# Performance work log

Measured on AMD Instinct MI355X. Metric: run time of the kernel, lower is better.

## Reference

```python
import jax, jax.numpy as jnp
import numpy as np

B, H, W, C = 2, 64, 64, 512
GROUPS = 32
EPS = 1e-5


def group_norm(x, gamma, beta):
    b, h, w, c = x.shape
    xg = x.reshape(b, h, w, GROUPS, c // GROUPS)
    mu = xg.mean(axis=(1, 2, 4), keepdims=True)
    var = xg.var(axis=(1, 2, 4), keepdims=True)
    xn = ((xg - mu) * jax.lax.rsqrt(var + EPS)).reshape(b, h, w, c)
    return xn * gamma + beta


def setup_inputs() -> dict:
    key = jax.random.key(0)
    ks = jax.random.split(key, 12)
    wscale = 0.02
    inputs = jax.random.normal(ks[0], (B, H, W, C), jnp.float32)
    gamma = jnp.ones((C,), jnp.float32)
    beta = jnp.zeros((C,), jnp.float32)
    Wq = jax.random.normal(ks[1], (C, C), jnp.float32) * wscale
    bq = jnp.zeros((C,), jnp.float32)
    Wk = jax.random.normal(ks[2], (C, C), jnp.float32) * wscale
    bk = jnp.zeros((C,), jnp.float32)
    Wv = jax.random.normal(ks[3], (C, C), jnp.float32) * wscale
    bv = jnp.zeros((C,), jnp.float32)
    Wp = jax.random.normal(ks[4], (C, C), jnp.float32) * wscale
    bp = jnp.zeros((C,), jnp.float32)
    return {"inputs": inputs, "gamma": gamma, "beta": beta,
            "Wq": Wq, "bq": bq, "Wk": Wk, "bk": bk,
            "Wv": Wv, "bv": bv, "Wp": Wp, "bp": bp}


def reference(inputs, gamma, beta, Wq, bq, Wk, bk, Wv, bv, Wp, bp):
    b, h, w, c = inputs.shape
    x = group_norm(inputs, gamma, beta)
    # QKV projections on [b, h, w, c], flatten spatial to sequence hw
    q = (x @ Wq + bq).reshape(b, h * w, c)
    k = (x @ Wk + bk).reshape(b, h * w, c)
    v = (x @ Wv + bv).reshape(b, h * w, c)
    scale = 1.0 / jnp.sqrt(jnp.asarray(c, q.dtype))
    # y[b,i,j] = <q_i, k_j> / sqrt(c); softmax over keys j (last axis, keras default)
    attn = jax.nn.softmax(jnp.einsum('bqc,bkc->bqk', q, k) * scale, axis=-1)
    # out_i = sum_j attn[i,j] * v_j  (matches v @ y^T in the original)
    o = jnp.einsum('bqk,bkc->bqc', attn, v).reshape(b, h, w, c)
    return (o @ Wp + bp) + inputs
```

## Files before the change

### kernel.cpp

```cpp
#include <hip/hip_runtime.h>
#include <hip/hip_bf16.h>
#include <hip/hip_cooperative_groups.h>
#include <cstddef>

namespace cg = cooperative_groups;


typedef __bf16 bf16;
typedef __attribute__((ext_vector_type(8))) __bf16 bf16x8;
typedef __attribute__((ext_vector_type(4))) __bf16 bf16x4;
typedef __attribute__((ext_vector_type(4))) float f32x4;

#define SEQ   4096
#define CCH   512
#define NBAT  2
#define NOMASK 0x7FFFFFFF
#define SMEM_BYTES 32768

__device__ __forceinline__ void prep_unit(
    char* smem, int bid, const float* __restrict__ x,
    const float* __restrict__ Wq, const float* __restrict__ Wk,
    const float* __restrict__ Wv, const float* __restrict__ Wp,
    const float* __restrict__ bq, const float* __restrict__ bk,
    const float* __restrict__ bv,
    float* __restrict__ statsP, bf16* __restrict__ WqkvT,
    bf16* __restrict__ WpT, float* __restrict__ biasQKV) {
    const int tid = threadIdx.x;
    if (bid < 512) {
        float* red = (float*)smem;
        int bg = bid >> 3, c = bid & 7;
        int b = bg >> 5, g = bg & 31;
        const float* base = x + (size_t)b * SEQ * CCH + g * 16;
        float s = 0.f, ss = 0.f;
        for (int i = tid; i < 2048; i += 256) {
            int sp = c * 512 + (i >> 2), q = i & 3;
            float4 v = *(const float4*)(base + (size_t)sp * CCH + q * 4);
            s  += v.x + v.y + v.z + v.w;
            ss += v.x * v.x + v.y * v.y + v.z * v.z + v.w * v.w;
        }
        #pragma unroll
        for (int o = 32; o > 0; o >>= 1) { s += __shfl_down(s, o); ss += __shfl_down(ss, o); }
        int wave = tid >> 6, lane = tid & 63;
        if (lane == 0) { red[wave] = s; red[4 + wave] = ss; }
        __syncthreads();
        if (tid == 0) {
            statsP[bg * 16 + c]     = red[0] + red[1] + red[2] + red[3];
            statsP[bg * 16 + 8 + c] = red[4] + red[5] + red[6] + red[7];
        }
        __syncthreads();
    } else if (bid < 1536) {
        float (*tile)[33] = (float(*)[33])smem;
        int w = bid - 512;
        int z = w >> 8, rest = w & 255;
        int k0 = (rest >> 4) * 32, n0 = (rest & 15) * 32;
        const float* W = (z == 0) ? Wq : (z == 1) ? Wk : (z == 2) ? Wv : Wp;
        int tx = tid & 31, ty = tid >> 5;
        #pragma unroll
        for (int i = ty; i < 32; i += 8)
            tile[i][tx] = W[(size_t)(k0 + i) * CCH + n0 + tx];
        __syncthreads();
        bf16* dst = (z < 3) ? (WqkvT + (size_t)z * CCH * CCH) : WpT;
        #pragma unroll
        for (int i = ty; i < 32; i += 8)
            dst[(size_t)(n0 + i) * CCH + k0 + tx] = (bf16)tile[tx][i];
        __syncthreads();
    } else {
        for (int i = tid; i < 1536; i += 256) {
            float v = (i < 512) ? bq[i] : (i < 1024) ? bk[i - 512] : bv[i - 1024];
            biasQKV[i] = v;
        }
    }
}

__device__ __forceinline__ void gn_table(char* smem, const float* __restrict__ statsP) {
    float* tbl = (float*)smem;
    const int tid = threadIdx.x;
    if (tid < 64) {
        float S = 0.f, SS = 0.f;
        #pragma unroll
        for (int c = 0; c < 8; ++c) { S += statsP[tid * 16 + c]; SS += statsP[tid * 16 + 8 + c]; }
        float mu = S * (1.f / 65536.f);
        float rs = rsqrtf(SS * (1.f / 65536.f) - mu * mu + 1e-5f);
        tbl[tid * 2] = mu; tbl[tid * 2 + 1] = rs;
    }
    __syncthreads();
}

__device__ __forceinline__ void gn_unit(
    char* smem, int w, const float* __restrict__ x,
    const float* __restrict__ gamma, const float* __restrict__ beta,
    bf16* __restrict__ xn) {
    const float* tbl = (const float*)smem;
    size_t idx = (size_t)w * 256 + threadIdx.x;
    int c4 = (int)(idx & 127);
    int b = (int)(idx >> 19);
    int bg = b * 32 + (c4 >> 2);
    float mu = tbl[bg * 2], rs = tbl[bg * 2 + 1];
    float4 v  = ((const float4*)x)[idx];
    float4 gm = ((const float4*)gamma)[c4];
    float4 bt = ((const float4*)beta)[c4];
    bf16x4 o;
    o[0] = (bf16)((v.x - mu) * rs * gm.x + bt.x);
    o[1] = (bf16)((v.y - mu) * rs * gm.y + bt.y);
    o[2] = (bf16)((v.z - mu) * rs * gm.z + bt.z);
    o[3] = (bf16)((v.w - mu) * rs * gm.w + bt.w);
    ((bf16x4*)xn)[idx] = o;
}

__device__ __forceinline__ void vtrans_unit(char* smem,
                                            const bf16* __restrict__ qkv,
                                            bf16* __restrict__ vT,
                                            int b, int s0, int c0) {
    bf16 (*tile)[65] = (bf16(*)[65])smem;
    const int tx = threadIdx.x & 63;
    const int w = threadIdx.x >> 6;
    #pragma unroll
    for (int i = 0; i < 16; ++i) {
        int row = w + i * 4;
        tile[row][tx] = qkv[((size_t)b * SEQ + s0 + row) * 1536 + 1024 + c0 + tx];
    }
    __syncthreads();
    #pragma unroll
    for (int i = 0; i < 16; ++i) {
        int row = w + i * 4;
        vT[((size_t)b * CCH + c0 + row) * SEQ + s0 + tx] = tile[tx][row];
    }
    __syncthreads();
}

template <int EPI, int BN>
__device__ __forceinline__ void gemm2_body(
    char* smem, int bxi, int byi, int bzi,
    const bf16* __restrict__ A, long long aBatch, int lda,
    const bf16* __restrict__ Bt, long long bBatch, int ldb,
    void* __restrict__ Cout, long long cBatch, int ldc,
    int K, int bkmask, float scale,
    const float* __restrict__ bias, const float* __restrict__ resid,
    float* __restrict__ lsum, long long lsumBatch) {
    constexpr int JN = BN / 32;
    bf16* As = (bf16*)smem;
    bf16* Bs = (bf16*)(smem + 16384);
    const int tid = threadIdx.x;
    const int lane = tid & 63;
    const int wave = tid >> 6;

    int zb = bzi, kc = 0;
    if constexpr (EPI == 2) { kc = zb & 1; zb >>= 1; }
    const long long m0 = (long long)bxi * 128;
    const long long n0 = (long long)byi * BN;
    const bf16* Ab = A + (long long)zb * aBatch + (EPI == 2 ? (long long)kc * 2048 : 0);
    const bf16* Bb = Bt + (long long)zb * bBatch + (EPI == 2 ? (long long)kc * 2048 : 0);

    const int wm = (wave & 1) * 64;
    const int wn = (wave >> 1) * (BN / 2);
    const int fm = lane & 15;
    const int q4 = lane >> 4;

    f32x4 acc[4][JN];
    #pragma unroll
    for (int i = 0; i < 4; ++i)
        #pragma unroll
        for (int j = 0; j < JN; ++j)
            acc[i][j] = (f32x4){0.f, 0.f, 0.f, 0.f};

    const int srow = tid >> 3;
    const int schunk = (tid & 7) ^ (srow & 7);

    for (int k0 = 0; k0 < K; k0 += 64) {
        const int kA = k0 + schunk * 8;
        const int kB = (k0 & bkmask) + schunk * 8;
        #pragma unroll
        for (int cb = 0; cb < 4; ++cb) {
            const bf16* g = Ab + (m0 + cb * 32 + srow) * (long long)lda + kA;
            __builtin_amdgcn_global_load_lds((const __attribute__((address_space(1))) void*)g,
                                             (__attribute__((address_space(3))) void*)&As[cb * 2048 + tid * 8], 16, 0, 0);
        }
        #pragma unroll
        for (int cb = 0; cb < BN / 32; ++cb) {
            const bf16* g = Bb + (n0 + cb * 32 + srow) * (long long)ldb + kB;
            __builtin_amdgcn_global_load_lds((const __attribute__((address_space(1))) void*)g,
                                             (__attribute__((address_space(3))) void*)&Bs[cb * 2048 + tid * 8], 16, 0, 0);
        }
        __syncthreads();
        #pragma unroll
        for (int kcc = 0; kcc < 2; ++kcc) {
            bf16x8 fa[4], fb[JN];
            #pragma unroll
            for (int i = 0; i < 4; ++i) {
                const int row = wm + i * 16 + fm;
                const int sw = ((kcc * 4 + q4) ^ (fm & 7)) * 8;
                fa[i] = *(const bf16x8*)&As[row * 64 + sw];
            }
            #pragma unroll
            for (int j = 0; j < JN; ++j) {
                const int row = wn + j * 16 + fm;
                const int sw = ((kcc * 4 + q4) ^ (fm & 7)) * 8;
                fb[j] = *(const bf16x8*)&Bs[row * 64 + sw];
            }
            #pragma unroll
            for (int i = 0; i < 4; ++i)
                #pragma unroll
                for (int j = 0; j < JN; ++j)
                    acc[i][j] = __builtin_amdgcn_mfma_f32_16x16x32_bf16(fa[i], fb[j], acc[i][j], 0, 0, 0);
        }
        __syncthreads();
    }

    float* lrow = (float*)(smem + 1024);
    if constexpr (EPI == 2) {
        float* lscr = (float*)smem;
        const float* lsb = lsum + (long long)zb * lsumBatch + m0;
        const int row = tid & 127, h = tid >> 7;
        float s = 0.f;
        #pragma unroll
        for (int p = 0; p < 32; ++p)
            s += lsb[(long long)(h * 32 + p) * SEQ + row];
        lscr[tid] = s;
        __syncthreads();
        if (tid < 128) lrow[tid] = 1.f / (lscr[tid] + lscr[tid + 128]);
        __syncthreads();
    }

    const int col = lane & 15;
    const int rowb = (lane >> 4) * 4;

    if constexpr (EPI == 1) {
        bf16* Pb = (bf16*)Cout + (long long)zb * cBatch;
        float* lsw = lsum + (long long)zb * lsumBatch
                   + ((long long)byi * 2 + (wave >> 1)) * SEQ;
        #pragma unroll
        for (int i = 0; i < 4; ++i) {
            float rs[4] = {0.f, 0.f, 0.f, 0.f};
            long long mg = m0 + wm + i * 16 + rowb;
            #pragma unroll
            for (int j = 0; j < JN; ++j) {
                long long ng = n0 + wn + j * 16 + col;
                #pragma unroll
                for (int r = 0; r < 4; ++r) {
                    float e = __expf(acc[i][j][r] * scale);
                    rs[r] += e;
                    Pb[(mg + r) * (long long)ldc + ng] = (bf16)e;
                }
            }
            #pragma unroll
            for (int r = 0; r < 4; ++r) {
                rs[r] += __shfl_xor(rs[r], 1);
                rs[r] += __shfl_xor(rs[r], 2);
                rs[r] += __shfl_xor(rs[r], 4);
                rs[r] += __shfl_xor(rs[r], 8);
            }
            if (col == 0) {
                #pragma unroll
                for (int r = 0; r < 4; ++r) lsw[mg + r] = rs[r];
            }
        }
    } else {
        #pragma unroll
        for (int i = 0; i < 4; ++i) {
            #pragma unroll
            for (int j = 0; j < JN; ++j) {
                long long mg = m0 + wm + i * 16 + rowb;
                long long ng = n0 + wn + j * 16 + col;
                #pragma unroll
                for (int r = 0; r < 4; ++r) {
                    float v = acc[i][j][r];
                    long long m = mg + r;
                    if constexpr (EPI == 0) {
                        ((bf16*)Cout)[m * (long long)ldc + ng] = (bf16)(v + bias[ng]);
                    } else if constexpr (EPI == 2) {
                        float inv = lrow[(int)(m - m0)];
                        ((bf16*)Cout)[(long long)zb * cBatch + m * (long long)ldc
                                      + kc * 512 + ng] = (bf16)(v * inv);
                    } else {
                        ((float*)Cout)[m * (long long)ldc + ng] =
                            v + bias[ng] + resid[m * CCH + ng];
                    }
                }
            }
        }
    }
}

struct FusedArgs {
    const float *x, *gamma, *beta, *Wq, *bq, *Wk, *bk, *Wv, *bv, *Wp, *bp;
    float* out;
    float* statsP; float* biasQKV; bf16* WqkvT; bf16* WpT; bf16* xn;
    float* lsum; bf16* qkv; bf16* o2; bf16* vT; bf16* P;
};

__global__ __launch_bounds__(256, 2) void fused(FusedArgs a) {
    cg::grid_group grid = cg::this_grid();
    __shared__ __align__(16) char smem[SMEM_BYTES];
    const int nb = gridDim.x;
    const float scale = 0.044194173824159216f;

    for (int w = blockIdx.x; w < 1537; w += nb)
        prep_unit(smem, w, a.x, a.Wq, a.Wk, a.Wv, a.Wp, a.bq, a.bk, a.bv,
                  a.statsP, a.WqkvT, a.WpT, a.biasQKV);
    grid.sync();

    gn_table(smem, a.statsP);
    for (int w = blockIdx.x; w < 4096; w += nb)
        gn_unit(smem, w, a.x, a.gamma, a.beta, a.xn);
    grid.sync();

    for (int w = blockIdx.x; w < 768; w += nb)
        gemm2_body<0, 128>(smem, w & 63, w >> 6, 0,
                           a.xn, 0, CCH, a.WqkvT, 0, CCH, a.qkv, 0, 1536,
                           CCH, NOMASK, 1.f, a.biasQKV, nullptr, nullptr, 0);
    grid.sync();

    for (int w = blockIdx.x; w < 3072; w += nb) {
        if (w < 1024) {
            int b = w >> 9, r = w & 511;
            vtrans_unit(smem, a.qkv, a.vT, b, (r >> 3) * 64, (r & 7) * 64);
        } else {
            int u = w - 1024;
            int bz = u >> 10, r = u & 1023;
            gemm2_body<1, 128>(smem, r >> 5, r & 31, bz,
                               a.qkv, (long long)SEQ * 1536, 1536,
                               a.qkv + 512, (long long)SEQ * 1536, 1536,
                               a.P, (long long)SEQ * SEQ, SEQ,
                               CCH, NOMASK, scale, nullptr, nullptr,
                               a.lsum, 64LL * SEQ);
        }
    }
    grid.sync();

    for (int w = blockIdx.x; w < 512; w += nb)
        gemm2_body<2, 128>(smem, w & 31, (w >> 5) & 3, w >> 7,
                           a.P, (long long)SEQ * SEQ, SEQ,
                           a.vT, (long long)CCH * SEQ, SEQ,
                           a.o2, (long long)SEQ * 1024, 1024,
                           2048, NOMASK, 1.f, nullptr, nullptr,
                           a.lsum, 64LL * SEQ);
    grid.sync();

    for (int w = blockIdx.x; w < 512; w += nb)
        gemm2_body<3, 64>(smem, w & 63, w >> 6, 0,
                          a.o2, 0, 1024, a.WpT, 0, CCH, a.out, 0, CCH,
                          1024, 511, 1.f, a.bp, a.x, nullptr, 0);
}

__global__ __launch_bounds__(256) void k_prep(
    const float* x, const float* Wq, const float* Wk, const float* Wv,
    const float* Wp, const float* bq, const float* bk, const float* bv,
    float* statsP, bf16* WqkvT, bf16* WpT, float* biasQKV) {
    __shared__ __align__(16) char smem[4352];
    prep_unit(smem, blockIdx.x, x, Wq, Wk, Wv, Wp, bq, bk, bv,
              statsP, WqkvT, WpT, biasQKV);
}

__global__ __launch_bounds__(256) void k_gn(
    const float* x, const float* statsP, const float* gamma,
    const float* beta, bf16* xn) {
    __shared__ __align__(16) char smem[512];
    gn_table(smem, statsP);
    gn_unit(smem, blockIdx.x, x, gamma, beta, xn);
}

template <int EPI, int BN>
__global__ __launch_bounds__(256, 2) void k_gemm2(
    const bf16* A, long long aBatch, int lda,
    const bf16* Bt, long long bBatch, int ldb,
    void* Cout, long long cBatch, int ldc,
    int K, int bkmask, float scale,
    const float* bias, const float* resid,
    float* lsum, long long lsumBatch) {
    __shared__ __align__(16) char smem[SMEM_BYTES];
    gemm2_body<EPI, BN>(smem, blockIdx.x, blockIdx.y, blockIdx.z,
                        A, aBatch, lda, Bt, bBatch, ldb, Cout, cBatch, ldc,
                        K, bkmask, scale, bias, resid, lsum, lsumBatch);
}

__global__ __launch_bounds__(256, 2) void k_qk_vtrans(
    const bf16* qkv, bf16* vT, bf16* P, float* lsum, float scale,
    int vtBlocks, long long qkBatch, long long pBatch, long long lsumBatch) {
    __shared__ __align__(16) char smem[SMEM_BYTES];
    const int bid = blockIdx.x;
    if (bid < vtBlocks) {
        int b = bid >> 9, r = bid & 511;
        vtrans_unit(smem, qkv, vT, b, (r >> 3) * 64, (r & 7) * 64);
    } else {
        int q = bid - vtBlocks;
        int bz = q >> 10, r = q & 1023;
        gemm2_body<1, 128>(smem, r >> 5, r & 31, bz,
                           qkv, qkBatch, 1536, qkv + 512, qkBatch, 1536,
                           P, pBatch, SEQ, CCH, NOMASK, scale,
                           nullptr, nullptr, lsum, lsumBatch);
    }
}

extern "C" void kernel_launch(void* const* d_in, const int* in_sizes, int n_in,
                              void* d_out, int out_size, void* d_ws, size_t ws_size,
                              hipStream_t stream) {
    const float* x     = (const float*)d_in[0];
    const float* gamma = (const float*)d_in[1];
    const float* beta  = (const float*)d_in[2];
    const float* Wq    = (const float*)d_in[3];
    const float* bq    = (const float*)d_in[4];
    const float* Wk    = (const float*)d_in[5];
    const float* bk    = (const float*)d_in[6];
    const float* Wv    = (const float*)d_in[7];
    const float* bv    = (const float*)d_in[8];
    const float* Wp    = (const float*)d_in[9];
    const float* bp    = (const float*)d_in[10];
    float* out = (float*)d_out;

    constexpr size_t OFF_STATS = 0;
    constexpr size_t OFF_BIAS  = 4096;
    constexpr size_t OFF_WQKVT = 12288;
    constexpr size_t OFF_WPT   = 1585152;
    constexpr size_t OFF_XN    = 2109440;
    constexpr size_t OFF_LSUM  = OFF_XN;
    constexpr size_t OFF_QKV   = 10498048;
    constexpr size_t OFF_O2    = OFF_QKV;
    constexpr size_t OFF_VT    = 35663872;
    constexpr size_t OFF_P     = 44052480;
    constexpr size_t NEED_FULL = OFF_P + (size_t)NBAT * SEQ * SEQ * 2;

    char* ws = (char*)d_ws;
    float* statsP  = (float*)(ws + OFF_STATS);
    float* biasQKV = (float*)(ws + OFF_BIAS);
    bf16*  WqkvT   = (bf16*)(ws + OFF_WQKVT);
    bf16*  WpT     = (bf16*)(ws + OFF_WPT);
    bf16*  xn      = (bf16*)(ws + OFF_XN);
    float* lsum    = (float*)(ws + OFF_LSUM);
    bf16*  qkv     = (bf16*)(ws + OFF_QKV);
    bf16*  o2      = (bf16*)(ws + OFF_O2);
    bf16*  vT      = (bf16*)(ws + OFF_VT);
    bf16*  P       = (bf16*)(ws + OFF_P);

    const float scale = 0.044194173824159216f;
    const bool full = ws_size >= NEED_FULL;

    bool coop = false;
    if (full) {
        int occ = 0;
        hipError_t oe = hipOccupancyMaxActiveBlocksPerMultiprocessor(
            &occ, (const void*)fused, 256, 0);
        if (oe == hipSuccess && occ >= 2) {
            FusedArgs a{x, gamma, beta, Wq, bq, Wk, bk, Wv, bv, Wp, bp, out,
                        statsP, biasQKV, WqkvT, WpT, xn, lsum, qkv, o2, vT, P};
            void* params[] = {&a};
            hipError_t le = hipLaunchCooperativeKernel(
                (const void*)fused, dim3(512), dim3(256), params, 0, stream);
            if (le == hipSuccess) coop = true;
            else (void)hipGetLastError();
        } else {
            (void)hipGetLastError();
        }
    }

    if (!coop) {
        k_prep<<<1537, 256, 0, stream>>>(x, Wq, Wk, Wv, Wp, bq, bk, bv,
                                         statsP, WqkvT, WpT, biasQKV);
        k_gn<<<4096, 256, 0, stream>>>(x, statsP, gamma, beta, xn);
        k_gemm2<0, 128><<<dim3(64, 12, 1), 256, 0, stream>>>(
            xn, 0, CCH, WqkvT, 0, CCH, qkv, 0, 1536,
            CCH, NOMASK, 1.f, biasQKV, nullptr, nullptr, 0);
        if (full) {
            k_qk_vtrans<<<3072, 256, 0, stream>>>(
                qkv, vT, P, lsum, scale, 1024,
                (long long)SEQ * 1536, (long long)SEQ * SEQ, 64LL * SEQ);
            k_gemm2<2, 128><<<dim3(32, 4, NBAT * 2), 256, 0, stream>>>(
                P, (long long)SEQ * SEQ, SEQ, vT, (long long)CCH * SEQ, SEQ,
                o2, (long long)SEQ * 1024, 1024,
                2048, NOMASK, 1.f, nullptr, nullptr, lsum, 64LL * SEQ);
        } else {
            for (int b = 0; b < NBAT; ++b) {
                const bf16* qb = qkv + (long long)b * SEQ * 1536;
                k_qk_vtrans<<<1536, 256, 0, stream>>>(
                    qb, vT + (long long)b * CCH * SEQ, P,
                    lsum + (long long)b * 64 * SEQ, scale, 512, 0, 0, 0);
                k_gemm2<2, 128><<<dim3(32, 4, 2), 256, 0, stream>>>(
                    P, 0, SEQ, vT + (long long)b * CCH * SEQ, 0, SEQ,
                    o2 + (long long)b * SEQ * 1024, 0, 1024,
                    2048, NOMASK, 1.f, nullptr, nullptr,
                    lsum + (long long)b * 64 * SEQ, 0);
            }
        }
        k_gemm2<3, 64><<<dim3(64, 8, 1), 256, 0, stream>>>(
            o2, 0, 1024, WpT, 0, CCH, out, 0, CCH,
            1024, 511, 1.f, bp, x, nullptr, 0);
    }
}
```

Before: 216.6 us.

## Replace cooperative launch with persistent kernel and custom atomic grid barrier

Swaps the cooperative-groups kernel and grid.sync for a regular launch of 1024 persistent blocks (4 per CU via launch bounds), synchronised by hand-written atomic counter barriers in workspace that are reset with a memset before each launch. The PV GEMM stage moves to 64-wide tiles with twice as many work units to fill the larger grid. The aim is to remove cooperative-launch overhead and raise occupancy. The risks are that the barrier deadlocks if not all 1024 blocks are co-resident, and that the 4-blocks-per-CU bound adds register pressure.

```diff
diff --git a/kernel.cpp b/kernel.cpp
--- a/kernel.cpp
+++ b/kernel.cpp
@@ -1,9 +1,6 @@
 #include <hip/hip_runtime.h>
 #include <hip/hip_bf16.h>
-#include <hip/hip_cooperative_groups.h>
 #include <cstddef>
-
-namespace cg = cooperative_groups;
 
 
 typedef __bf16 bf16;
@@ -16,6 +13,21 @@
 #define NBAT  2
 #define NOMASK 0x7FFFFFFF
 #define SMEM_BYTES 32768
+#define PGRID 1024
+
+__device__ __forceinline__ void grid_bar(unsigned* bar, int idx) {
+    __syncthreads();
+    if (threadIdx.x == 0) {
+        __threadfence();
+        __hip_atomic_fetch_add(&bar[idx], 1u, __ATOMIC_RELEASE,
+                               __HIP_MEMORY_SCOPE_AGENT);
+        while (__hip_atomic_load(&bar[idx], __ATOMIC_RELAXED,
+                                 __HIP_MEMORY_SCOPE_AGENT) < (unsigned)PGRID)
+            __builtin_amdgcn_s_sleep(1);
+        __threadfence();
+    }
+    __syncthreads();
+}
 
 __device__ __forceinline__ void prep_unit(
     char* smem, int bid, const float* __restrict__ x,
@@ -286,29 +298,29 @@
     float* out;
     float* statsP; float* biasQKV; bf16* WqkvT; bf16* WpT; bf16* xn;
     float* lsum; bf16* qkv; bf16* o2; bf16* vT; bf16* P;
+    unsigned* bar;
 };
 
-__global__ __launch_bounds__(256, 2) void fused(FusedArgs a) {
-    cg::grid_group grid = cg::this_grid();
+__global__ __launch_bounds__(256, 4) void persistent(FusedArgs a) {
     __shared__ __align__(16) char smem[SMEM_BYTES];
-    const int nb = gridDim.x;
+    const int nb = PGRID;
     const float scale = 0.044194173824159216f;
 
     for (int w = blockIdx.x; w < 1537; w += nb)
         prep_unit(smem, w, a.x, a.Wq, a.Wk, a.Wv, a.Wp, a.bq, a.bk, a.bv,
                   a.statsP, a.WqkvT, a.WpT, a.biasQKV);
-    grid.sync();
+    grid_bar(a.bar, 0);
 
     gn_table(smem, a.statsP);
     for (int w = blockIdx.x; w < 4096; w += nb)
         gn_unit(smem, w, a.x, a.gamma, a.beta, a.xn);
-    grid.sync();
+    grid_bar(a.bar, 1);
 
     for (int w = blockIdx.x; w < 768; w += nb)
         gemm2_body<0, 128>(smem, w & 63, w >> 6, 0,
                            a.xn, 0, CCH, a.WqkvT, 0, CCH, a.qkv, 0, 1536,
                            CCH, NOMASK, 1.f, a.biasQKV, nullptr, nullptr, 0);
-    grid.sync();
+    grid_bar(a.bar, 2);
 
     for (int w = blockIdx.x; w < 3072; w += nb) {
         if (w < 1024) {
@@ -325,16 +337,16 @@
                                a.lsum, 64LL * SEQ);
         }
     }
-    grid.sync();
-
-    for (int w = blockIdx.x; w < 512; w += nb)
-        gemm2_body<2, 128>(smem, w & 31, (w >> 5) & 3, w >> 7,
-                           a.P, (long long)SEQ * SEQ, SEQ,
-                           a.vT, (long long)CCH * SEQ, SEQ,
-                           a.o2, (long long)SEQ * 1024, 1024,
-                           2048, NOMASK, 1.f, nullptr, nullptr,
-                           a.lsum, 64LL * SEQ);
-    grid.sync();
+    grid_bar(a.bar, 3);
+
+    for (int w = blockIdx.x; w < 1024; w += nb)
+        gemm2_body<2, 64>(smem, w & 31, (w >> 5) & 7, w >> 8,
+                          a.P, (long long)SEQ * SEQ, SEQ,
+                          a.vT, (long long)CCH * SEQ, SEQ,
+                          a.o2, (long long)SEQ * 1024, 1024,
+                          2048, NOMASK, 1.f, nullptr, nullptr,
+                          a.lsum, 64LL * SEQ);
+    grid_bar(a.bar, 4);
 
     for (int w = blockIdx.x; w < 512; w += nb)
         gemm2_body<3, 64>(smem, w & 63, w >> 6, 0,
@@ -409,6 +421,7 @@
 
     constexpr size_t OFF_STATS = 0;
     constexpr size_t OFF_BIAS  = 4096;
+    constexpr size_t OFF_BAR   = 10240;
     constexpr size_t OFF_WQKVT = 12288;
     constexpr size_t OFF_WPT   = 1585152;
     constexpr size_t OFF_XN    = 2109440;
@@ -422,6 +435,7 @@
     char* ws = (char*)d_ws;
     float* statsP  = (float*)(ws + OFF_STATS);
     float* biasQKV = (float*)(ws + OFF_BIAS);
+    unsigned* bar  = (unsigned*)(ws + OFF_BAR);
     bf16*  WqkvT   = (bf16*)(ws + OFF_WQKVT);
     bf16*  WpT     = (bf16*)(ws + OFF_WPT);
     bf16*  xn      = (bf16*)(ws + OFF_XN);
@@ -434,25 +448,21 @@
     const float scale = 0.044194173824159216f;
     const bool full = ws_size >= NEED_FULL;
 
-    bool coop = false;
+    bool usePersist = false;
     if (full) {
         int occ = 0;
         hipError_t oe = hipOccupancyMaxActiveBlocksPerMultiprocessor(
-            &occ, (const void*)fused, 256, 0);
-        if (oe == hipSuccess && occ >= 2) {
-            FusedArgs a{x, gamma, beta, Wq, bq, Wk, bk, Wv, bv, Wp, bp, out,
-                        statsP, biasQKV, WqkvT, WpT, xn, lsum, qkv, o2, vT, P};
-            void* params[] = {&a};
-            hipError_t le = hipLaunchCooperativeKernel(
-                (const void*)fused, dim3(512), dim3(256), params, 0, stream);
-            if (le == hipSuccess) coop = true;
-            else (void)hipGetLastError();
-        } else {
-            (void)hipGetLastError();
-        }
-    }
-
-    if (!coop) {
+            &occ, (const void*)persistent, 256, 0);
+        usePersist = (oe == hipSuccess && occ >= 4);
+        if (!usePersist) (void)hipGetLastError();
+    }
+
+    if (usePersist) {
+        hipMemsetAsync(ws + OFF_BAR, 0, 64, stream);
+        FusedArgs a{x, gamma, beta, Wq, bq, Wk, bk, Wv, bv, Wp, bp, out,
+                    statsP, biasQKV, WqkvT, WpT, xn, lsum, qkv, o2, vT, P, bar};
+        persistent<<<PGRID, 256, 0, stream>>>(a);
+    } else {
         k_prep<<<1537, 256, 0, stream>>>(x, Wq, Wk, Wv, Wp, bq, bk, bv,
                                          statsP, WqkvT, WpT, biasQKV);
         k_gn<<<4096, 256, 0, stream>>>(x, statsP, gamma, beta, xn);
```

Measured after the change: 211.2 us. 2.5% less time.

## Fold output projection into V and fuse PV with bias and residual

Applied to the files above, without the earlier changes.

Precomputes (V·Wp)^T as a GEMM alongside the QK^T scores kernel, replacing the V transpose. The PV GEMM then writes the final output directly, applying softmax normalization, bias and residual, and the separate output-projection GEMM and the o2 intermediate go away. The split-K PV launch over two halves is replaced by a full-K pass with narrower N tiles. The cooperative persistent fused kernel with grid syncs is dropped in favour of plain launches. The cost is an extra V·Wp GEMM and a longer K loop per PV block with fewer blocks.

```diff
diff --git a/kernel.cpp b/kernel.cpp
--- a/kernel.cpp
+++ b/kernel.cpp
@@ -1,9 +1,6 @@
 #include <hip/hip_runtime.h>
 #include <hip/hip_bf16.h>
-#include <hip/hip_cooperative_groups.h>
 #include <cstddef>
-
-namespace cg = cooperative_groups;
 
 
 typedef __bf16 bf16;
@@ -14,7 +11,6 @@
 #define SEQ   4096
 #define CCH   512
 #define NBAT  2
-#define NOMASK 0x7FFFFFFF
 #define SMEM_BYTES 32768
 
 __device__ __forceinline__ void prep_unit(
@@ -72,8 +68,20 @@
     }
 }
 
-__device__ __forceinline__ void gn_table(char* smem, const float* __restrict__ statsP) {
-    float* tbl = (float*)smem;
+__global__ __launch_bounds__(256) void k_prep(
+    const float* x, const float* Wq, const float* Wk, const float* Wv,
+    const float* Wp, const float* bq, const float* bk, const float* bv,
+    float* statsP, bf16* WqkvT, bf16* WpT, float* biasQKV) {
+    __shared__ __align__(16) char smem[4352];
+    prep_unit(smem, blockIdx.x, x, Wq, Wk, Wv, Wp, bq, bk, bv,
+              statsP, WqkvT, WpT, biasQKV);
+}
+
+__global__ __launch_bounds__(256) void k_gn(
+    const float* __restrict__ x, const float* __restrict__ statsP,
+    const float* __restrict__ gamma, const float* __restrict__ beta,
+    bf16* __restrict__ xn) {
+    __shared__ float tbl[128];
     const int tid = threadIdx.x;
     if (tid < 64) {
         float S = 0.f, SS = 0.f;
@@ -84,14 +92,7 @@
         tbl[tid * 2] = mu; tbl[tid * 2 + 1] = rs;
     }
     __syncthreads();
-}
-
-__device__ __forceinline__ void gn_unit(
-    char* smem, int w, const float* __restrict__ x,
-    const float* __restrict__ gamma, const float* __restrict__ beta,
-    bf16* __restrict__ xn) {
-    const float* tbl = (const float*)smem;
-    size_t idx = (size_t)w * 256 + threadIdx.x;
+    size_t idx = (size_t)blockIdx.x * 256 + tid;
     int c4 = (int)(idx & 127);
     int b = (int)(idx >> 19);
     int bg = b * 32 + (c4 >> 2);
@@ -107,34 +108,13 @@
     ((bf16x4*)xn)[idx] = o;
 }
 
-__device__ __forceinline__ void vtrans_unit(char* smem,
-                                            const bf16* __restrict__ qkv,
-                                            bf16* __restrict__ vT,
-                                            int b, int s0, int c0) {
-    bf16 (*tile)[65] = (bf16(*)[65])smem;
-    const int tx = threadIdx.x & 63;
-    const int w = threadIdx.x >> 6;
-    #pragma unroll
-    for (int i = 0; i < 16; ++i) {
-        int row = w + i * 4;
-        tile[row][tx] = qkv[((size_t)b * SEQ + s0 + row) * 1536 + 1024 + c0 + tx];
-    }
-    __syncthreads();
-    #pragma unroll
-    for (int i = 0; i < 16; ++i) {
-        int row = w + i * 4;
-        vT[((size_t)b * CCH + c0 + row) * SEQ + s0 + tx] = tile[tx][row];
-    }
-    __syncthreads();
-}
-
 template <int EPI, int BN>
 __device__ __forceinline__ void gemm2_body(
-    char* smem, int bxi, int byi, int bzi,
+    char* smem, int bxi, int byi, int zb,
     const bf16* __restrict__ A, long long aBatch, int lda,
     const bf16* __restrict__ Bt, long long bBatch, int ldb,
     void* __restrict__ Cout, long long cBatch, int ldc,
-    int K, int bkmask, float scale,
+    int K, float scale,
     const float* __restrict__ bias, const float* __restrict__ resid,
     float* __restrict__ lsum, long long lsumBatch) {
     constexpr int JN = BN / 32;
@@ -144,12 +124,10 @@
     const int lane = tid & 63;
     const int wave = tid >> 6;
 
-    int zb = bzi, kc = 0;
-    if constexpr (EPI == 2) { kc = zb & 1; zb >>= 1; }
     const long long m0 = (long long)bxi * 128;
     const long long n0 = (long long)byi * BN;
-    const bf16* Ab = A + (long long)zb * aBatch + (EPI == 2 ? (long long)kc * 2048 : 0);
-    const bf16* Bb = Bt + (long long)zb * bBatch + (EPI == 2 ? (long long)kc * 2048 : 0);
+    const bf16* Ab = A + (long long)zb * aBatch;
+    const bf16* Bb = Bt + (long long)zb * bBatch;
 
     const int wm = (wave & 1) * 64;
     const int wn = (wave >> 1) * (BN / 2);
@@ -167,17 +145,16 @@
     const int schunk = (tid & 7) ^ (srow & 7);
 
     for (int k0 = 0; k0 < K; k0 += 64) {
-        const int kA = k0 + schunk * 8;
-        const int kB = (k0 & bkmask) + schunk * 8;
+        const int kk = k0 + schunk * 8;
         #pragma unroll
         for (int cb = 0; cb < 4; ++cb) {
-            const bf16* g = Ab + (m0 + cb * 32 + srow) * (long long)lda + kA;
+            const bf16* g = Ab + (m0 + cb * 32 + srow) * (long long)lda + kk;
             __builtin_amdgcn_global_load_lds((const __attribute__((address_space(1))) void*)g,
                                              (__attribute__((address_space(3))) void*)&As[cb * 2048 + tid * 8], 16, 0, 0);
         }
         #pragma unroll
         for (int cb = 0; cb < BN / 32; ++cb) {
-            const bf16* g = Bb + (n0 + cb * 32 + srow) * (long long)ldb + kB;
+            const bf16* g = Bb + (n0 + cb * 32 + srow) * (long long)ldb + kk;
             __builtin_amdgcn_global_load_lds((const __attribute__((address_space(1))) void*)g,
                                              (__attribute__((address_space(3))) void*)&Bs[cb * 2048 + tid * 8], 16, 0, 0);
         }
@@ -265,15 +242,14 @@
                 for (int r = 0; r < 4; ++r) {
                     float v = acc[i][j][r];
                     long long m = mg + r;
+                    long long cidx = (long long)zb * cBatch + m * (long long)ldc + ng;
                     if constexpr (EPI == 0) {
-                        ((bf16*)Cout)[m * (long long)ldc + ng] = (bf16)(v + bias[ng]);
+                        ((bf16*)Cout)[cidx] = (bf16)(v + bias[ng]);
                     } else if constexpr (EPI == 2) {
                         float inv = lrow[(int)(m - m0)];
-                        ((bf16*)Cout)[(long long)zb * cBatch + m * (long long)ldc
-                                      + kc * 512 + ng] = (bf16)(v * inv);
+                        ((float*)Cout)[cidx] = v * inv + bias[ng] + resid[cidx];
                     } else {
-                        ((float*)Cout)[m * (long long)ldc + ng] =
-                            v + bias[ng] + resid[m * CCH + ng];
+                        ((bf16*)Cout)[cidx] = (bf16)v;
                     }
                 }
             }
@@ -281,114 +257,44 @@
     }
 }
 
-struct FusedArgs {
-    const float *x, *gamma, *beta, *Wq, *bq, *Wk, *bk, *Wv, *bv, *Wp, *bp;
-    float* out;
-    float* statsP; float* biasQKV; bf16* WqkvT; bf16* WpT; bf16* xn;
-    float* lsum; bf16* qkv; bf16* o2; bf16* vT; bf16* P;
-};
-
-__global__ __launch_bounds__(256, 2) void fused(FusedArgs a) {
-    cg::grid_group grid = cg::this_grid();
+__global__ __launch_bounds__(256, 2) void k_qkv(
+    const bf16* xn, const bf16* WqkvT, const float* biasQKV, bf16* qkv) {
     __shared__ __align__(16) char smem[SMEM_BYTES];
-    const int nb = gridDim.x;
-    const float scale = 0.044194173824159216f;
-
-    for (int w = blockIdx.x; w < 1537; w += nb)
-        prep_unit(smem, w, a.x, a.Wq, a.Wk, a.Wv, a.Wp, a.bq, a.bk, a.bv,
-                  a.statsP, a.WqkvT, a.WpT, a.biasQKV);
-    grid.sync();
-
-    gn_table(smem, a.statsP);
-    for (int w = blockIdx.x; w < 4096; w += nb)
-        gn_unit(smem, w, a.x, a.gamma, a.beta, a.xn);
-    grid.sync();
-
-    for (int w = blockIdx.x; w < 768; w += nb)
-        gemm2_body<0, 128>(smem, w & 63, w >> 6, 0,
-                           a.xn, 0, CCH, a.WqkvT, 0, CCH, a.qkv, 0, 1536,
-                           CCH, NOMASK, 1.f, a.biasQKV, nullptr, nullptr, 0);
-    grid.sync();
-
-    for (int w = blockIdx.x; w < 3072; w += nb) {
-        if (w < 1024) {
-            int b = w >> 9, r = w & 511;
-            vtrans_unit(smem, a.qkv, a.vT, b, (r >> 3) * 64, (r & 7) * 64);
-        } else {
-            int u = w - 1024;
-            int bz = u >> 10, r = u & 1023;
-            gemm2_body<1, 128>(smem, r >> 5, r & 31, bz,
-                               a.qkv, (long long)SEQ * 1536, 1536,
-                               a.qkv + 512, (long long)SEQ * 1536, 1536,
-                               a.P, (long long)SEQ * SEQ, SEQ,
-                               CCH, NOMASK, scale, nullptr, nullptr,
-                               a.lsum, 64LL * SEQ);
-        }
-    }
-    grid.sync();
-
-    for (int w = blockIdx.x; w < 512; w += nb)
-        gemm2_body<2, 128>(smem, w & 31, (w >> 5) & 3, w >> 7,
-                           a.P, (long long)SEQ * SEQ, SEQ,
-                           a.vT, (long long)CCH * SEQ, SEQ,
-                           a.o2, (long long)SEQ * 1024, 1024,
-                           2048, NOMASK, 1.f, nullptr, nullptr,
-                           a.lsum, 64LL * SEQ);
-    grid.sync();
-
-    for (int w = blockIdx.x; w < 512; w += nb)
-        gemm2_body<3, 64>(smem, w & 63, w >> 6, 0,
-                          a.o2, 0, 1024, a.WpT, 0, CCH, a.out, 0, CCH,
-                          1024, 511, 1.f, a.bp, a.x, nullptr, 0);
-}
-
-__global__ __launch_bounds__(256) void k_prep(
-    const float* x, const float* Wq, const float* Wk, const float* Wv,
-    const float* Wp, const float* bq, const float* bk, const float* bv,
-    float* statsP, bf16* WqkvT, bf16* WpT, float* biasQKV) {
-    __shared__ __align__(16) char smem[4352];
-    prep_unit(smem, blockIdx.x, x, Wq, Wk, Wv, Wp, bq, bk, bv,
-              statsP, WqkvT, WpT, biasQKV);
-}
-
-__global__ __launch_bounds__(256) void k_gn(
-    const float* x, const float* statsP, const float* gamma,
-    const float* beta, bf16* xn) {
-    __shared__ __align__(16) char smem[512];
-    gn_table(smem, statsP);
-    gn_unit(smem, blockIdx.x, x, gamma, beta, xn);
-}
-
-template <int EPI, int BN>
-__global__ __launch_bounds__(256, 2) void k_gemm2(
-    const bf16* A, long long aBatch, int lda,
-    const bf16* Bt, long long bBatch, int ldb,
-    void* Cout, long long cBatch, int ldc,
-    int K, int bkmask, float scale,
-    const float* bias, const float* resid,
+    gemm2_body<0, 128>(smem, blockIdx.x, blockIdx.y, 0,
+                       xn, 0, CCH, WqkvT, 0, CCH, qkv, 0, 1536,
+                       CCH, 1.f, biasQKV, nullptr, nullptr, 0);
+}
+
+__global__ __launch_bounds__(256, 2) void k_qk_vpt(
+    const bf16* qkv, const bf16* WpT, bf16* vpT, bf16* P, float* lsum,
+    float scale, int nQK, long long qkBatch, long long pBatch,
+    long long lsumBatch, long long vptBatch) {
+    __shared__ __align__(16) char smem[SMEM_BYTES];
+    const int u = blockIdx.x;
+    if (u < nQK) {
+        int bz = u >> 10, r = u & 1023;
+        gemm2_body<1, 128>(smem, r >> 5, r & 31, bz,
+                           qkv, qkBatch, 1536, qkv + 512, qkBatch, 1536,
+                           P, pBatch, SEQ, CCH, scale,
+                           nullptr, nullptr, lsum, lsumBatch);
+    } else {
+        int w = u - nQK;
+        int bz = w >> 7, rr = w & 127;
+        gemm2_body<5, 128>(smem, rr >> 5, rr & 31, bz,
+                           WpT, 0, CCH, qkv + 1024, qkBatch, 1536,
+                           vpT, vptBatch, SEQ, CCH, 1.f,
+                           nullptr, nullptr, nullptr, 0);
+    }
+}
+
+__global__ __launch_bounds__(256, 2) void k_pv(
+    const bf16* P, long long pBatch, const bf16* vpT, long long vptBatch,
+    const float* bp, const float* x, float* out, long long oBatch,
     float* lsum, long long lsumBatch) {
     __shared__ __align__(16) char smem[SMEM_BYTES];
-    gemm2_body<EPI, BN>(smem, blockIdx.x, blockIdx.y, blockIdx.z,
-                        A, aBatch, lda, Bt, bBatch, ldb, Cout, cBatch, ldc,
-                        K, bkmask, scale, bias, resid, lsum, lsumBatch);
-}
-
-__global__ __launch_bounds__(256, 2) void k_qk_vtrans(
-    const bf16* qkv, bf16* vT, bf16* P, float* lsum, float scale,
-    int vtBlocks, long long qkBatch, long long pBatch, long long lsumBatch) {
-    __shared__ __align__(16) char smem[SMEM_BYTES];
-    const int bid = blockIdx.x;
-    if (bid < vtBlocks) {
-        int b = bid >> 9, r = bid & 511;
-        vtrans_unit(smem, qkv, vT, b, (r >> 3) * 64, (r & 7) * 64);
-    } else {
-        int q = bid - vtBlocks;
-        int bz = q >> 10, r = q & 1023;
-        gemm2_body<1, 128>(smem, r >> 5, r & 31, bz,
-                           qkv, qkBatch, 1536, qkv + 512, qkBatch, 1536,
-                           P, pBatch, SEQ, CCH, NOMASK, scale,
-                           nullptr, nullptr, lsum, lsumBatch);
-    }
+    gemm2_body<2, 64>(smem, blockIdx.x, blockIdx.y, blockIdx.z,
+                      P, pBatch, SEQ, vpT, vptBatch, SEQ,
+                      out, oBatch, CCH, SEQ, 1.f, bp, x, lsum, lsumBatch);
 }
 
 extern "C" void kernel_launch(void* const* d_in, const int* in_sizes, int n_in,
@@ -414,8 +320,7 @@
     constexpr size_t OFF_XN    = 2109440;
     constexpr size_t OFF_LSUM  = OFF_XN;
     constexpr size_t OFF_QKV   = 10498048;
-    constexpr size_t OFF_O2    = OFF_QKV;
-    constexpr size_t OFF_VT    = 35663872;
+    constexpr size_t OFF_VPT   = 35663872;
     constexpr size_t OFF_P     = 44052480;
     constexpr size_t NEED_FULL = OFF_P + (size_t)NBAT * SEQ * SEQ * 2;
 
@@ -427,61 +332,35 @@
     bf16*  xn      = (bf16*)(ws + OFF_XN);
     float* lsum    = (float*)(ws + OFF_LSUM);
     bf16*  qkv     = (bf16*)(ws + OFF_QKV);
-    bf16*  o2      = (bf16*)(ws + OFF_O2);
-    bf16*  vT      = (bf16*)(ws + OFF_VT);
+    bf16*  vpT     = (bf16*)(ws + OFF_VPT);
     bf16*  P       = (bf16*)(ws + OFF_P);
 
     const float scale = 0.044194173824159216f;
     const bool full = ws_size >= NEED_FULL;
 
-    bool coop = false;
+    k_prep<<<1537, 256, 0, stream>>>(x, Wq, Wk, Wv, Wp, bq, bk, bv,
+                                     statsP, WqkvT, WpT, biasQKV);
+    k_gn<<<4096, 256, 0, stream>>>(x, statsP, gamma, beta, xn);
+    k_qkv<<<dim3(64, 12), 256, 0, stream>>>(xn, WqkvT, biasQKV, qkv);
+
     if (full) {
-        int occ = 0;
-        hipError_t oe = hipOccupancyMaxActiveBlocksPerMultiprocessor(
-            &occ, (const void*)fused, 256, 0);
-        if (oe == hipSuccess && occ >= 2) {
-            FusedArgs a{x, gamma, beta, Wq, bq, Wk, bk, Wv, bv, Wp, bp, out,
-                        statsP, biasQKV, WqkvT, WpT, xn, lsum, qkv, o2, vT, P};
-            void* params[] = {&a};
-            hipError_t le = hipLaunchCooperativeKernel(
-                (const void*)fused, dim3(512), dim3(256), params, 0, stream);
-            if (le == hipSuccess) coop = true;
-            else (void)hipGetLastError();
-        } else {
-            (void)hipGetLastError();
-        }
-    }
-
-    if (!coop) {
-        k_prep<<<1537, 256, 0, stream>>>(x, Wq, Wk, Wv, Wp, bq, bk, bv,
-                                         statsP, WqkvT, WpT, biasQKV);
-        k_gn<<<4096, 256, 0, stream>>>(x, statsP, gamma, beta, xn);
-        k_gemm2<0, 128><<<dim3(64, 12, 1), 256, 0, stream>>>(
-            xn, 0, CCH, WqkvT, 0, CCH, qkv, 0, 1536,
-            CCH, NOMASK, 1.f, biasQKV, nullptr, nullptr, 0);
-        if (full) {
-            k_qk_vtrans<<<3072, 256, 0, stream>>>(
-                qkv, vT, P, lsum, scale, 1024,
-                (long long)SEQ * 1536, (long long)SEQ * SEQ, 64LL * SEQ);
-            k_gemm2<2, 128><<<dim3(32, 4, NBAT * 2), 256, 0, stream>>>(
-                P, (long long)SEQ * SEQ, SEQ, vT, (long long)CCH * SEQ, SEQ,
-                o2, (long long)SEQ * 1024, 1024,
-                2048, NOMASK, 1.f, nullptr, nullptr, lsum, 64LL * SEQ);
-        } else {
-            for (int b = 0; b < NBAT; ++b) {
-                const bf16* qb = qkv + (long long)b * SEQ * 1536;
-                k_qk_vtrans<<<1536, 256, 0, stream>>>(
-                    qb, vT + (long long)b * CCH * SEQ, P,
-                    lsum + (long long)b * 64 * SEQ, scale, 512, 0, 0, 0);
-                k_gemm2<2, 128><<<dim3(32, 4, 2), 256, 0, stream>>>(
-                    P, 0, SEQ, vT + (long long)b * CCH * SEQ, 0, SEQ,
-                    o2 + (long long)b * SEQ * 1024, 0, 1024,
-                    2048, NOMASK, 1.f, nullptr, nullptr,
-                    lsum + (long long)b * 64 * SEQ, 0);
-            }
-        }
-        k_gemm2<3, 64><<<dim3(64, 8, 1), 256, 0, stream>>>(
-            o2, 0, 1024, WpT, 0, CCH, out, 0, CCH,
-            1024, 511, 1.f, bp, x, nullptr, 0);
-    }
-}
+        k_qk_vpt<<<2304, 256, 0, stream>>>(
+            qkv, WpT, vpT, P, lsum, scale, 2048,
+            (long long)SEQ * 1536, (long long)SEQ * SEQ, 64LL * SEQ,
+            (long long)CCH * SEQ);
+        k_pv<<<dim3(32, 8, NBAT), 256, 0, stream>>>(
+            P, (long long)SEQ * SEQ, vpT, (long long)CCH * SEQ,
+            bp, x, out, (long long)SEQ * CCH, lsum, 64LL * SEQ);
+    } else {
+        for (int b = 0; b < NBAT; ++b) {
+            const bf16* qkvb = qkv + (long long)b * SEQ * 1536;
+            bf16* vptb = vpT + (long long)b * CCH * SEQ;
+            float* lsumb = lsum + (long long)b * 64 * SEQ;
+            k_qk_vpt<<<1152, 256, 0, stream>>>(
+                qkvb, WpT, vptb, P, lsumb, scale, 1024, 0, 0, 0, 0);
+            k_pv<<<dim3(32, 8, 1), 256, 0, stream>>>(
+                P, 0, vptb, 0, bp, x + (long long)b * SEQ * CCH,
+                out + (long long)b * SEQ * CCH, 0, lsumb, 0);
+        }
+    }
+}
```

New measurement: 217.1 us. About the same (+0.2%).
